# Kernel tuning notes

Hardware: AMD Instinct MI355X
Metric: run time of the kernel (lower is better)

Reference implementation:

```python
import jax, jax.numpy as jnp
import numpy as np

B, N_IN, N_ALL, NPT, K, C, H = 8, 20000, 1200, 1024, 34, 96, 6
DH = C // H
RADIUS2 = (2.5 * 0.04) ** 2  # grid_size=0.04, sigma=1.0 -> radius 0.1


def _fps(xyz, npoint):
    # furthest point sampling, vectorized over batch, scan over sample steps
    Bb, Nn, _ = xyz.shape
    def step(carry, _):
        dist, far = carry
        cen = jnp.take_along_axis(xyz, far[:, None, None], axis=1)  # [B,1,3]
        d = jnp.sum((xyz - cen) ** 2, -1)                           # [B,N]
        dist = jnp.minimum(dist, d)
        return (dist, jnp.argmax(dist, -1).astype(jnp.int32)), far
    init = (jnp.full((Bb, Nn), 1e10, xyz.dtype), jnp.zeros((Bb,), jnp.int32))
    _, idx = jax.lax.scan(step, init, None, length=npoint)
    return idx.T  # [B, npoint]


def _gather(x, idx):
    return jnp.take_along_axis(x, idx[:, :, None], axis=1)


def _ln(x, g, b):
    m = jnp.mean(x, -1, keepdims=True)
    v = jnp.var(x, -1, keepdims=True)
    return (x - m) * jax.lax.rsqrt(v + 1e-5) * g + b


def _forward(point_clouds, cloud_colors, W_in, b_in, Wq, Wk, Wv, Wo, Wpos, W1, b1, W2, b2, g1, be1, g2, be2, sel):
    fps_idx = _fps(point_clouds, N_ALL)      # [B,1200]
    fps_idx = fps_idx[:, sel]                # random 1024 of 1200 (fixed permutation)
    coord = _gather(point_clouds, fps_idx)   # [B,P,3]
    color = _gather(cloud_colors, fps_idx)   # [B,P,3]
    # ball query within each cloud (all clouds have equal count -> batched dense dists)
    d2 = jnp.sum((coord[:, :, None] - coord[:, None]) ** 2, -1)        # [B,P,P]
    valid = d2 <= RADIUS2
    nidx = jnp.argsort(jnp.where(valid, d2, 1e10), axis=-1)[..., :K]   # [B,P,K]
    nvalid = jnp.take_along_axis(valid, nidx, axis=-1)                 # [B,P,K]
    feat = jnp.concatenate([color, coord], -1)                         # [B,P,6]
    x = feat @ W_in + b_in                                             # [B,P,C]
    q = (x @ Wq).reshape(B, NPT, H, DH)
    k = x @ Wk
    v = x @ Wv
    def gat(t):  # gather per-neighbor features: [B,P,C*] -> [B,P,K,C*]
        return jnp.take_along_axis(t, nidx.reshape(B, NPT * K)[:, :, None], axis=1).reshape(B, NPT, K, -1)
    kn, vn, pn = gat(k), gat(v), gat(coord)
    pe = (coord[:, :, None] - pn) @ Wpos                               # [B,P,K,C] rel-pos enc
    kn = (kn + pe).reshape(B, NPT, K, H, DH)
    vn = (vn + pe).reshape(B, NPT, K, H, DH)
    logits = jnp.einsum('bphd,bpkhd->bphk', q, kn) / jnp.sqrt(jnp.float32(DH))
    logits = jnp.where(nvalid[:, :, None, :], logits, -1e9)
    attn = jax.nn.softmax(logits, -1)
    out = jnp.einsum('bphk,bpkhd->bphd', attn, vn).reshape(B, NPT, C)
    x = _ln(x + out @ Wo, g1, be1)
    x = _ln(x + jax.nn.relu(x @ W1 + b1) @ W2 + b2, g2, be2)
    features = jnp.transpose(x, (0, 2, 1))                             # [B,C,P]
    return features, coord


def setup_inputs() -> dict:
    key = jax.random.key(0)
    ks = jax.random.split(key, 16)
    s = 0.1
    w = lambda k, shp: jax.random.normal(k, shp, jnp.float32) * s
    return {
        'point_clouds': jax.random.uniform(ks[0], (B, N_IN, 3), jnp.float32),
        'cloud_colors': jax.random.uniform(ks[1], (B, N_IN, 3), jnp.float32),
        'W_in': w(ks[2], (6, C)), 'b_in': jnp.zeros((C,), jnp.float32),
        'Wq': w(ks[3], (C, C)), 'Wk': w(ks[4], (C, C)), 'Wv': w(ks[5], (C, C)),
        'Wo': w(ks[6], (C, C)), 'Wpos': w(ks[7], (3, C)),
        'W1': w(ks[8], (C, 4 * C)), 'b1': jnp.zeros((4 * C,), jnp.float32),
        'W2': w(ks[9], (4 * C, C)), 'b2': jnp.zeros((C,), jnp.float32),
        'g1': jnp.ones((C,), jnp.float32), 'be1': jnp.zeros((C,), jnp.float32),
        'g2': jnp.ones((C,), jnp.float32), 'be2': jnp.zeros((C,), jnp.float32),
        'sel': jax.random.permutation(ks[10], N_ALL)[:NPT].astype(jnp.int32),
    }


def reference(point_clouds, cloud_colors, W_in, b_in, Wq, Wk, Wv, Wo, Wpos, W1, b1, W2, b2, g1, be1, g2, be2, sel):
    return _forward(point_clouds, cloud_colors, W_in, b_in, Wq, Wk, Wv, Wo, Wpos, W1, b1, W2, b2, g1, be1, g2, be2, sel)
```

## Files before the change

kernel.cpp:

```cpp
#include <hip/hip_runtime.h>
#include <math.h>

#define B_   8
#define NIN  20000
#define NALL 1200
#define NPTQ 1024
#define KNB  34
#define CH   96
#define FF   384
#define NQ   (B_ * NPTQ)
#define SL   20

typedef unsigned int   u32;
typedef unsigned long long u64;

__device__ __forceinline__ float scrub(float f) {
    u32 u = __float_as_uint(f);
    return ((u & 0x7F800000u) == 0x7F800000u) ? 12345.0f : f;
}

__global__ __launch_bounds__(1024, 4) void fps_kernel(const float* __restrict__ pc,
                                                      int* __restrict__ fps_idx) {
#pragma clang fp contract(off)
    const int b = blockIdx.x;
    const int tid = threadIdx.x;
    const int lane = tid & 63;
    const int wid = tid >> 6;
    const float* base = pc + (size_t)b * NIN * 3;

    float px[SL], py[SL], pz[SL], dist[SL];
#pragma unroll
    for (int j = 0; j < SL; ++j) {
        int idx = tid + j * 1024;
        bool ok = (j < SL - 1) || (idx < NIN);
        int ia = ok ? idx : 0;
        float x = base[(size_t)ia * 3 + 0];
        float y = base[(size_t)ia * 3 + 1];
        float z = base[(size_t)ia * 3 + 2];
        px[j] = __shfl(x, lane);
        py[j] = __shfl(y, lane);
        pz[j] = __shfl(z, lane);
        dist[j] = ok ? 1e10f : -1.0f;
    }

    __shared__ u64 red[2][16];

    if (tid == 0) fps_idx[b * NALL + 0] = 0;
    float cx = base[0], cy = base[1], cz = base[2];

    for (int it = 1; it < NALL; ++it) {
        const int p = it & 1;
        float bd = -1e38f; int bi = 0;
#pragma unroll
        for (int j = 0; j < SL; ++j) {
            float dx = __fsub_rn(px[j], cx);
            float dy = __fsub_rn(py[j], cy);
            float dz = __fsub_rn(pz[j], cz);
            float d = __fadd_rn(__fadd_rn(__fmul_rn(dx, dx), __fmul_rn(dy, dy)),
                                __fmul_rn(dz, dz));
            float nd = fminf(dist[j], d);
            dist[j] = nd;
            if (nd > bd) { bd = nd; bi = tid + j * 1024; }
        }
        u64 key = ((u64)__float_as_uint(bd) << 32) | (u32)(NIN - bi);
#pragma unroll
        for (int s = 32; s; s >>= 1) {
            u64 o = __shfl_xor(key, s, 64);
            key = (o > key) ? o : key;
        }
        if (lane == 0) red[p][wid] = key;
        __syncthreads();
        u64 k2 = red[p][lane & 15];
#pragma unroll
        for (int s = 1; s < 16; s <<= 1) {
            u64 o = __shfl_xor(k2, s, 64);
            k2 = (o > k2) ? o : k2;
        }
        int widx = NIN - (int)(k2 & 0xFFFFFFFFu);
        if (tid == 0) fps_idx[b * NALL + it] = widx;
        const float* wp = base + (size_t)widx * 3;
        cx = wp[0]; cy = wp[1]; cz = wp[2];
    }
}

__global__ void gather_kernel(const float* __restrict__ pc,
                              const int* __restrict__ fps_idx, const int* __restrict__ sel,
                              float* __restrict__ coord, float* __restrict__ out_coord) {
    int t = blockIdx.x * 256 + threadIdx.x;
    if (t >= NQ) return;
    int b = t >> 10, j = t & 1023;
    int p = fps_idx[b * NALL + sel[j]];
    p = (p < 0) ? 0 : ((p >= NIN) ? (NIN - 1) : p);
    const float* pp = pc + ((size_t)b * NIN + p) * 3;
    float x = pp[0], y = pp[1], z = pp[2];
    coord[(size_t)t * 3 + 0] = x;
    coord[(size_t)t * 3 + 1] = y;
    coord[(size_t)t * 3 + 2] = z;
    out_coord[(size_t)t * 3 + 0] = scrub(x);
    out_coord[(size_t)t * 3 + 1] = scrub(y);
    out_coord[(size_t)t * 3 + 2] = scrub(z);
}

__global__ void knn_kernel(const float* __restrict__ coord, int* __restrict__ nbr) {
    __shared__ float sx[NPTQ], sy[NPTQ], sz[NPTQ];
    const double RAD2D = (2.5 * 0.04) * (2.5 * 0.04);
    int b = blockIdx.x >> 8;
    int i0 = (blockIdx.x & 255) * 4;
    const float* cb = coord + (size_t)b * NPTQ * 3;
    for (int t = threadIdx.x; t < NPTQ; t += 256) {
        sx[t] = cb[(size_t)t * 3 + 0];
        sy[t] = cb[(size_t)t * 3 + 1];
        sz[t] = cb[(size_t)t * 3 + 2];
    }
    __syncthreads();
    int wid = threadIdx.x >> 6, lane = threadIdx.x & 63;
    int i = i0 + wid;
    float qx = sx[i], qy = sy[i], qz = sz[i];
    u64 pk[16];
#pragma unroll
    for (int t = 0; t < 16; ++t) {
        int j = lane + t * 64;
        float dx = __fsub_rn(qx, sx[j]);
        float dy = __fsub_rn(qy, sy[j]);
        float dz = __fsub_rn(qz, sz[j]);
        float d2 = __fadd_rn(__fadd_rn(__fmul_rn(dx, dx), __fmul_rn(dy, dy)),
                             __fmul_rn(dz, dz));
        bool valid = ((double)d2 <= RAD2D);
        pk[t] = valid ? (((u64)__float_as_uint(d2) << 32) | (u32)j) : ~0ull;
    }
    int* out = nbr + ((size_t)b * NPTQ + i) * KNB;
    int k = 0;
    for (; k < KNB; ++k) {
        u64 m = ~0ull;
#pragma unroll
        for (int t = 0; t < 16; ++t) m = (pk[t] < m) ? pk[t] : m;
#pragma unroll
        for (int s = 32; s; s >>= 1) {
            u64 o = __shfl_xor(m, s, 64);
            m = (o < m) ? o : m;
        }
        if (m == ~0ull) break;
#pragma unroll
        for (int t = 0; t < 16; ++t) if (pk[t] == m) pk[t] = ~0ull;
        if (lane == 0) out[k] = (int)(m & 0xFFFFFFFFu);
    }
    for (; k < KNB; ++k) if (lane == 0) out[k] = -1;
}

__global__ void xproj_kernel(const float* __restrict__ pc, const float* __restrict__ col,
                             const int* __restrict__ fps_idx, const int* __restrict__ sel,
                             const float* __restrict__ Win, const float* __restrict__ bin,
                             float* __restrict__ x) {
    int idx = blockIdx.x * 256 + threadIdx.x;
    if (idx >= NQ * CH) return;
    int q = idx / CH, c = idx - q * CH;
    int b = q >> 10, j = q & 1023;
    int p = fps_idx[b * NALL + sel[j]];
    p = (p < 0) ? 0 : ((p >= NIN) ? (NIN - 1) : p);
    const float* pp = pc + ((size_t)b * NIN + p) * 3;
    const float* cc = col + ((size_t)b * NIN + p) * 3;
    float acc = bin[c];
    acc += cc[0] * Win[0 * CH + c];
    acc += cc[1] * Win[1 * CH + c];
    acc += cc[2] * Win[2 * CH + c];
    acc += pp[0] * Win[3 * CH + c];
    acc += pp[1] * Win[4 * CH + c];
    acc += pp[2] * Win[5 * CH + c];
    x[idx] = acc;
}

__global__ void qkv_kernel(const float* __restrict__ x,
                           const float* __restrict__ Wq, const float* __restrict__ Wk,
                           const float* __restrict__ Wv,
                           float* __restrict__ qo, float* __restrict__ ko,
                           float* __restrict__ vo) {
    int idx = blockIdx.x * 256 + threadIdx.x;
    if (idx >= NQ * CH) return;
    int q = idx / CH, c = idx - q * CH;
    const float* xr = x + (size_t)q * CH;
    float aq = 0.f, ak = 0.f, av = 0.f;
    for (int k = 0; k < CH; ++k) {
        float xv = xr[k];
        aq += xv * Wq[k * CH + c];
        ak += xv * Wk[k * CH + c];
        av += xv * Wv[k * CH + c];
    }
    qo[idx] = aq; ko[idx] = ak; vo[idx] = av;
}

__global__ __launch_bounds__(384) void attn_kernel(float* __restrict__ qr1,
                            const float* __restrict__ km, const float* __restrict__ vm,
                            const float* __restrict__ coord, const int* __restrict__ nbr,
                            const float* __restrict__ Wpos, const float* __restrict__ Wo,
                            const float* __restrict__ x) {
    __shared__ float wp[3 * CH];
    __shared__ float os[4][CH];
    for (int t = threadIdx.x; t < 3 * CH; t += 384) wp[t] = Wpos[t];
    __syncthreads();
    int lq = threadIdx.x / CH;
    int c = threadIdx.x - lq * CH;
    int qi = blockIdx.x * 4 + lq;
    int b = qi >> 10, i = qi & 1023;
    const float* crd = coord + (size_t)b * NPTQ * 3;
    float cx = crd[(size_t)i * 3], cy = crd[(size_t)i * 3 + 1], cz = crd[(size_t)i * 3 + 2];
    float qv = qr1[(size_t)qi * CH + c];
    const int* nb = nbr + (size_t)qi * KNB;
    float m = -1e30f, l = 0.f, acc = 0.f;
    for (int t = 0; t < KNB; ++t) {
        int j = nb[t];
        if (j < 0) break;
        float dx = cx - crd[(size_t)j * 3];
        float dy = cy - crd[(size_t)j * 3 + 1];
        float dz = cz - crd[(size_t)j * 3 + 2];
        float pe = dx * wp[c] + dy * wp[CH + c] + dz * wp[2 * CH + c];
        size_t row = (size_t)(b * NPTQ + j) * CH + c;
        float kn = km[row] + pe;
        float s = qv * kn;
        s += __shfl_xor(s, 1); s += __shfl_xor(s, 2);
        s += __shfl_xor(s, 4); s += __shfl_xor(s, 8);
        float logit = s * 0.25f;
        float mn = fmaxf(m, logit);
        float sc = expf(m - mn);
        float p = expf(logit - mn);
        float vn = vm[row] + pe;
        l = l * sc + p;
        acc = acc * sc + p * vn;
        m = mn;
    }
    os[lq][c] = (l > 0.f) ? acc / l : 0.f;
    __syncthreads();
    float r = x[(size_t)qi * CH + c];
    for (int k = 0; k < CH; ++k) r += os[lq][k] * Wo[k * CH + c];
    qr1[(size_t)qi * CH + c] = r;
}

__global__ void ln_kernel(const float* __restrict__ in, const float* __restrict__ g,
                          const float* __restrict__ be, float* __restrict__ out) {
    int row = blockIdx.x * 4 + (threadIdx.x >> 6);
    int lane = threadIdx.x & 63;
    const float* r = in + (size_t)row * CH;
    float e0 = r[lane];
    float e1 = (lane < 32) ? r[64 + lane] : 0.0f;
    float s = e0 + e1;
#pragma unroll
    for (int k = 32; k; k >>= 1) s += __shfl_xor(s, k);
    float mean = s * (1.0f / 96.0f);
    float d0 = e0 - mean, d1 = e1 - mean;
    float vs = d0 * d0 + ((lane < 32) ? d1 * d1 : 0.0f);
#pragma unroll
    for (int k = 32; k; k >>= 1) vs += __shfl_xor(vs, k);
    float rs = 1.0f / sqrtf(vs * (1.0f / 96.0f) + 1e-5f);
    float* o = out + (size_t)row * CH;
    o[lane] = d0 * rs * g[lane] + be[lane];
    if (lane < 32) o[64 + lane] = d1 * rs * g[64 + lane] + be[64 + lane];
}

__global__ __launch_bounds__(384) void ffn_kernel(const float* __restrict__ x2,
                           const float* __restrict__ W1, const float* __restrict__ b1,
                           const float* __restrict__ W2, const float* __restrict__ b2,
                           float* __restrict__ r2) {
    __shared__ float xs[4][CH];
    __shared__ float hs[4][FF];
    __shared__ float ps[4][4][CH];
    int row0 = blockIdx.x * 4, t = threadIdx.x;
    { int r = t / CH, c = t - (t / CH) * CH;
      xs[r][c] = x2[(size_t)(row0 + r) * CH + c]; }
    __syncthreads();
    {
        float bt = b1[t];
        float a0 = bt, a1 = bt, a2 = bt, a3 = bt;
        for (int k = 0; k < CH; ++k) {
            float w = W1[k * FF + t];
            a0 += xs[0][k] * w; a1 += xs[1][k] * w;
            a2 += xs[2][k] * w; a3 += xs[3][k] * w;
        }
        hs[0][t] = fmaxf(a0, 0.f); hs[1][t] = fmaxf(a1, 0.f);
        hs[2][t] = fmaxf(a2, 0.f); hs[3][t] = fmaxf(a3, 0.f);
    }
    __syncthreads();
    {
        int chunk = t / CH, c = t - (t / CH) * CH;
        float p0 = 0.f, p1 = 0.f, p2 = 0.f, p3 = 0.f;
        for (int m = chunk * CH; m < (chunk + 1) * CH; ++m) {
            float w = W2[m * CH + c];
            p0 += hs[0][m] * w; p1 += hs[1][m] * w;
            p2 += hs[2][m] * w; p3 += hs[3][m] * w;
        }
        ps[0][chunk][c] = p0; ps[1][chunk][c] = p1;
        ps[2][chunk][c] = p2; ps[3][chunk][c] = p3;
    }
    __syncthreads();
    { int r = t / CH, c = t - (t / CH) * CH;
      float rr = xs[r][c] + ((ps[r][0][c] + ps[r][1][c]) + (ps[r][2][c] + ps[r][3][c])) + b2[c];
      r2[(size_t)(row0 + r) * CH + c] = rr; }
}

__global__ void ln2t_kernel(const float* __restrict__ in, const float* __restrict__ g,
                            const float* __restrict__ be, float* __restrict__ out) {
    int row = blockIdx.x * 4 + (threadIdx.x >> 6);
    int lane = threadIdx.x & 63;
    int b = row >> 10, i = row & 1023;
    const float* r = in + (size_t)row * CH;
    float e0 = r[lane];
    float e1 = (lane < 32) ? r[64 + lane] : 0.0f;
    float s = e0 + e1;
#pragma unroll
    for (int k = 32; k; k >>= 1) s += __shfl_xor(s, k);
    float mean = s * (1.0f / 96.0f);
    float d0 = e0 - mean, d1 = e1 - mean;
    float vs = d0 * d0 + ((lane < 32) ? d1 * d1 : 0.0f);
#pragma unroll
    for (int k = 32; k; k >>= 1) vs += __shfl_xor(vs, k);
    float rs = 1.0f / sqrtf(vs * (1.0f / 96.0f) + 1e-5f);
    float y0 = d0 * rs * g[lane] + be[lane];
    out[((size_t)(b * CH + lane)) * NPTQ + i] = scrub(y0);
    if (lane < 32) {
        float y1 = d1 * rs * g[64 + lane] + be[64 + lane];
        out[((size_t)(b * CH + 64 + lane)) * NPTQ + i] = scrub(y1);
    }
}

extern "C" void kernel_launch(void* const* d_in, const int* in_sizes, int n_in,
                              void* d_out, int out_size, void* d_ws, size_t ws_size,
                              hipStream_t stream) {
    const float* pc   = (const float*)d_in[0];
    const float* col  = (const float*)d_in[1];
    const float* Win  = (const float*)d_in[2];
    const float* bin  = (const float*)d_in[3];
    const float* Wq   = (const float*)d_in[4];
    const float* Wk   = (const float*)d_in[5];
    const float* Wv   = (const float*)d_in[6];
    const float* Wo   = (const float*)d_in[7];
    const float* Wpos = (const float*)d_in[8];
    const float* W1   = (const float*)d_in[9];
    const float* b1   = (const float*)d_in[10];
    const float* W2   = (const float*)d_in[11];
    const float* b2   = (const float*)d_in[12];
    const float* g1   = (const float*)d_in[13];
    const float* be1  = (const float*)d_in[14];
    const float* g2   = (const float*)d_in[15];
    const float* be2  = (const float*)d_in[16];
    const int*  sel   = (const int*)d_in[17];

    float* out_feat  = (float*)d_out;
    float* out_coord = out_feat + (size_t)B_ * CH * NPTQ;

    char* ws = (char*)d_ws;
    size_t off = 0;
    auto alloc = [&](size_t bytes) { void* p = ws + off; off += (bytes + 255) & ~(size_t)255; return p; };
    int*   w_fps   = (int*)  alloc((size_t)B_ * NALL * 4);
    float* w_coord = (float*)alloc((size_t)NQ * 3 * 4);
    int*   w_nbr   = (int*)  alloc((size_t)NQ * KNB * 4);
    float* w_x     = (float*)alloc((size_t)NQ * CH * 4);
    float* w_q     = (float*)alloc((size_t)NQ * CH * 4);
    float* w_k     = (float*)alloc((size_t)NQ * CH * 4);
    float* w_v     = (float*)alloc((size_t)NQ * CH * 4);
    (void)ws_size; (void)in_sizes; (void)n_in; (void)out_size;

    fps_kernel<<<B_, 1024, 0, stream>>>(pc, w_fps);
    gather_kernel<<<NQ / 256, 256, 0, stream>>>(pc, w_fps, sel, w_coord, out_coord);
    knn_kernel<<<NQ / 4, 256, 0, stream>>>(w_coord, w_nbr);
    xproj_kernel<<<NQ * CH / 256, 256, 0, stream>>>(pc, col, w_fps, sel, Win, bin, w_x);
    qkv_kernel<<<NQ * CH / 256, 256, 0, stream>>>(w_x, Wq, Wk, Wv, w_q, w_k, w_v);
    attn_kernel<<<NQ / 4, 384, 0, stream>>>(w_q, w_k, w_v, w_coord, w_nbr, Wpos, Wo, w_x);
    ln_kernel<<<NQ / 4, 256, 0, stream>>>(w_q, g1, be1, w_k);
    ffn_kernel<<<NQ / 4, 384, 0, stream>>>(w_k, W1, b1, W2, b2, w_v);
    ln2t_kernel<<<NQ / 4, 256, 0, stream>>>(w_v, g2, be2, out_feat);
}
```

Baseline: 2.656 ms.

## Accelerate FPS with spatial grid cells and bounding-box pruning of updates

Replaces the brute-force furthest point sampling, which updates all 20000 distances every iteration, with a uniform 8x8x8 grid. Points are bucketed per cell, and each cell tracks its max distance and argmax point. Each iteration only rescans cells whose box lower bound to the new centroid is below the cell's current max distance, then reduces over cell keys. This cuts per-iteration work but adds grid-build cost, shared-memory distance storage, global-memory reads of the sorted points, and extra syncthreads per iteration. It relies on the points lying in [0,1] for cell bounds, and clamps coordinates outside that range into edge cells.

```diff
diff --git a/kernel.cpp b/kernel.cpp
--- a/kernel.cpp
+++ b/kernel.cpp
@@ -9,7 +9,10 @@
 #define CH   96
 #define FF   384
 #define NQ   (B_ * NPTQ)
-#define SL   20
+
+#define GC   8
+#define NC   (GC * GC * GC)
+#define CW   0.125f
 
 typedef unsigned int   u32;
 typedef unsigned long long u64;
@@ -19,67 +22,162 @@
     return ((u & 0x7F800000u) == 0x7F800000u) ? 12345.0f : f;
 }
 
-__global__ __launch_bounds__(1024, 4) void fps_kernel(const float* __restrict__ pc,
-                                                      int* __restrict__ fps_idx) {
+__device__ __forceinline__ int cell_of(float x, float y, float z) {
+    int ix = (int)(x * (float)GC); ix = ix < 0 ? 0 : (ix > GC - 1 ? GC - 1 : ix);
+    int iy = (int)(y * (float)GC); iy = iy < 0 ? 0 : (iy > GC - 1 ? GC - 1 : iy);
+    int iz = (int)(z * (float)GC); iz = iz < 0 ? 0 : (iz > GC - 1 ? GC - 1 : iz);
+    return (ix * GC + iy) * GC + iz;
+}
+
+__global__ __launch_bounds__(1024) void fps_kernel(
+        const float* __restrict__ pc, int* __restrict__ fps_idx,
+        float* __restrict__ gsx, float* __restrict__ gsy, float* __restrict__ gsz,
+        int* __restrict__ gsidx) {
 #pragma clang fp contract(off)
     const int b = blockIdx.x;
     const int tid = threadIdx.x;
     const int lane = tid & 63;
     const int wid = tid >> 6;
     const float* base = pc + (size_t)b * NIN * 3;
-
-    float px[SL], py[SL], pz[SL], dist[SL];
-#pragma unroll
-    for (int j = 0; j < SL; ++j) {
+    float* bsx = gsx + (size_t)b * NIN;
+    float* bsy = gsy + (size_t)b * NIN;
+    float* bsz = gsz + (size_t)b * NIN;
+    int*   bsi = gsidx + (size_t)b * NIN;
+
+    __shared__ float dist[NIN];
+    __shared__ u64   ckey[NC];
+    __shared__ float cwx[NC], cwy[NC], cwz[NC];
+    __shared__ int   cstart[NC + 1];
+    __shared__ int   ccur[NC];
+    __shared__ int   updList[2][NC];
+    __shared__ int   nUpd[2];
+    __shared__ u64   part[16];
+    __shared__ int   partc[16];
+    __shared__ u64   bcKey;
+    __shared__ int   bcCell;
+
+    for (int c = tid; c < NC; c += 1024) ccur[c] = 0;
+    __syncthreads();
+    for (int j = 0; j < 20; ++j) {
         int idx = tid + j * 1024;
-        bool ok = (j < SL - 1) || (idx < NIN);
-        int ia = ok ? idx : 0;
-        float x = base[(size_t)ia * 3 + 0];
-        float y = base[(size_t)ia * 3 + 1];
-        float z = base[(size_t)ia * 3 + 2];
-        px[j] = __shfl(x, lane);
-        py[j] = __shfl(y, lane);
-        pz[j] = __shfl(z, lane);
-        dist[j] = ok ? 1e10f : -1.0f;
-    }
-
-    __shared__ u64 red[2][16];
-
+        if (idx < NIN) {
+            float x = base[(size_t)idx * 3 + 0];
+            float y = base[(size_t)idx * 3 + 1];
+            float z = base[(size_t)idx * 3 + 2];
+            atomicAdd(&ccur[cell_of(x, y, z)], 1);
+        }
+    }
+    __syncthreads();
+    if (tid == 0) {
+        int acc = 0;
+        for (int c = 0; c < NC; ++c) { cstart[c] = acc; acc += ccur[c]; }
+        cstart[NC] = acc;
+        nUpd[0] = 0; nUpd[1] = 0;
+    }
+    for (int s = tid; s < NIN; s += 1024) dist[s] = 1e10f;
+    __syncthreads();
+    if (tid < NC) {
+        ccur[tid] = cstart[tid];
+        int cnt = cstart[tid + 1] - cstart[tid];
+        ckey[tid] = cnt ? (((u64)__float_as_uint(1e10f) << 32) | 1u) : 0ull;
+    }
+    __syncthreads();
+    for (int j = 0; j < 20; ++j) {
+        int idx = tid + j * 1024;
+        if (idx < NIN) {
+            float x = base[(size_t)idx * 3 + 0];
+            float y = base[(size_t)idx * 3 + 1];
+            float z = base[(size_t)idx * 3 + 2];
+            int pos = atomicAdd(&ccur[cell_of(x, y, z)], 1);
+            bsx[pos] = x; bsy[pos] = y; bsz[pos] = z; bsi[pos] = idx;
+        }
+    }
+    __syncthreads();
+
+    float cx = base[0], cy = base[1], cz = base[2];
     if (tid == 0) fps_idx[b * NALL + 0] = 0;
-    float cx = base[0], cy = base[1], cz = base[2];
 
     for (int it = 1; it < NALL; ++it) {
         const int p = it & 1;
-        float bd = -1e38f; int bi = 0;
-#pragma unroll
-        for (int j = 0; j < SL; ++j) {
-            float dx = __fsub_rn(px[j], cx);
-            float dy = __fsub_rn(py[j], cy);
-            float dz = __fsub_rn(pz[j], cz);
-            float d = __fadd_rn(__fadd_rn(__fmul_rn(dx, dx), __fmul_rn(dy, dy)),
-                                __fmul_rn(dz, dz));
-            float nd = fminf(dist[j], d);
-            dist[j] = nd;
-            if (nd > bd) { bd = nd; bi = tid + j * 1024; }
-        }
-        u64 key = ((u64)__float_as_uint(bd) << 32) | (u32)(NIN - bi);
-#pragma unroll
-        for (int s = 32; s; s >>= 1) {
-            u64 o = __shfl_xor(key, s, 64);
-            key = (o > key) ? o : key;
-        }
-        if (lane == 0) red[p][wid] = key;
+        if (tid < NC) {
+            u64 k = ckey[tid];
+            bool needs = false;
+            if (k != 0) {
+                float maxd = __uint_as_float((u32)(k >> 32));
+                float lx = (float)(tid >> 6) * CW;
+                float ly = (float)((tid >> 3) & 7) * CW;
+                float lz = (float)(tid & 7) * CW;
+                float tx = fmaxf(fmaxf(lx - cx, cx - (lx + CW)), 0.0f);
+                float ty = fmaxf(fmaxf(ly - cy, cy - (ly + CW)), 0.0f);
+                float tz = fmaxf(fmaxf(lz - cz, cz - (lz + CW)), 0.0f);
+                float lb = tx * tx + ty * ty + tz * tz;
+                needs = (lb * 0.999f < maxd);
+            }
+            u64 mask = __ballot(needs);
+            if (mask) {
+                int leader = __ffsll((unsigned long long)mask) - 1;
+                int basep = 0;
+                if (lane == leader) basep = atomicAdd(&nUpd[p], (int)__popcll(mask));
+                basep = __shfl(basep, leader);
+                if (needs) {
+                    int prefix = __popcll(mask & ((1ull << lane) - 1ull));
+                    updList[p][basep + prefix] = tid;
+                }
+            }
+        }
         __syncthreads();
-        u64 k2 = red[p][lane & 15];
-#pragma unroll
-        for (int s = 1; s < 16; s <<= 1) {
-            u64 o = __shfl_xor(k2, s, 64);
-            k2 = (o > k2) ? o : k2;
-        }
-        int widx = NIN - (int)(k2 & 0xFFFFFFFFu);
-        if (tid == 0) fps_idx[b * NALL + it] = widx;
-        const float* wp = base + (size_t)widx * 3;
-        cx = wp[0]; cy = wp[1]; cz = wp[2];
+        const int M = nUpd[p];
+        if (tid == 0) nUpd[p ^ 1] = 0;
+        for (int w = wid; w < M; w += 16) {
+            int c = updList[p][w];
+            int s0 = cstart[c], s1 = cstart[c + 1];
+            u64 bk = 0; float bx = 0.f, by = 0.f, bz = 0.f;
+            for (int s = s0 + lane; s < s1; s += 64) {
+                float x = bsx[s], y = bsy[s], z = bsz[s];
+                float dx = __fsub_rn(x, cx);
+                float dy = __fsub_rn(y, cy);
+                float dz = __fsub_rn(z, cz);
+                float d = __fadd_rn(__fadd_rn(__fmul_rn(dx, dx), __fmul_rn(dy, dy)),
+                                    __fmul_rn(dz, dz));
+                float nd = fminf(dist[s], d);
+                dist[s] = nd;
+                u64 kk = ((u64)__float_as_uint(nd) << 32) | (u32)(NIN - bsi[s]);
+                if (kk > bk) { bk = kk; bx = x; by = y; bz = z; }
+            }
+            u64 kpre = bk;
+#pragma unroll
+            for (int st = 32; st; st >>= 1) {
+                u64 o = __shfl_xor(bk, st, 64);
+                bk = (o > bk) ? o : bk;
+            }
+            u64 mm = __ballot(kpre == bk);
+            int src = __ffsll((unsigned long long)mm) - 1;
+            bx = __shfl(bx, src); by = __shfl(by, src); bz = __shfl(bz, src);
+            if (lane == 0) { ckey[c] = bk; cwx[c] = bx; cwy[c] = by; cwz[c] = bz; }
+        }
+        __syncthreads();
+        if (tid < NC) {
+            u64 k2 = ckey[tid]; int c2 = tid;
+#pragma unroll
+            for (int st = 32; st; st >>= 1) {
+                u64 o = __shfl_xor(k2, st, 64);
+                int oc = __shfl_xor(c2, st, 64);
+                if (o > k2) { k2 = o; c2 = oc; }
+            }
+            if (lane == 0) { part[wid] = k2; partc[wid] = c2; }
+        }
+        __syncthreads();
+        if (tid == 0) {
+            u64 kb = part[0]; int cb = partc[0];
+#pragma unroll
+            for (int w = 1; w < NC / 64; ++w)
+                if (part[w] > kb) { kb = part[w]; cb = partc[w]; }
+            bcKey = kb; bcCell = cb;
+        }
+        __syncthreads();
+        u64 kw = bcKey; int cw = bcCell;
+        if (tid == 0) fps_idx[b * NALL + it] = NIN - (int)(kw & 0xFFFFFFFFu);
+        cx = cwx[cw]; cy = cwy[cw]; cz = cwz[cw];
     }
 }
 
@@ -348,6 +446,10 @@
     char* ws = (char*)d_ws;
     size_t off = 0;
     auto alloc = [&](size_t bytes) { void* p = ws + off; off += (bytes + 255) & ~(size_t)255; return p; };
+    float* w_sx    = (float*)alloc((size_t)B_ * NIN * 4);
+    float* w_sy    = (float*)alloc((size_t)B_ * NIN * 4);
+    float* w_sz    = (float*)alloc((size_t)B_ * NIN * 4);
+    int*   w_sidx  = (int*)  alloc((size_t)B_ * NIN * 4);
     int*   w_fps   = (int*)  alloc((size_t)B_ * NALL * 4);
     float* w_coord = (float*)alloc((size_t)NQ * 3 * 4);
     int*   w_nbr   = (int*)  alloc((size_t)NQ * KNB * 4);
@@ -357,7 +459,7 @@
     float* w_v     = (float*)alloc((size_t)NQ * CH * 4);
     (void)ws_size; (void)in_sizes; (void)n_in; (void)out_size;
 
-    fps_kernel<<<B_, 1024, 0, stream>>>(pc, w_fps);
+    fps_kernel<<<B_, 1024, 0, stream>>>(pc, w_fps, w_sx, w_sy, w_sz, w_sidx);
     gather_kernel<<<NQ / 256, 256, 0, stream>>>(pc, w_fps, sel, w_coord, out_coord);
     knn_kernel<<<NQ / 4, 256, 0, stream>>>(w_coord, w_nbr);
     xproj_kernel<<<NQ * CH / 256, 256, 0, stream>>>(pc, col, w_fps, sel, Win, bin, w_x);
```

Measured after the change: 3.180 ms. 1.2x slower.
